# Kernel tuning notes

Measured on AMD Instinct MI355X. Metric: run time of the kernel, lower is better.

Reference implementation:

```python
import jax, jax.numpy as jnp
import numpy as np

B, T, D_MODEL = 1, 2048, 4096
NUM_Q_HEADS, NUM_KV_HEADS, KEY_SIZE = 32, 8, 128
ATTN_MULT = 0.08838834764831845  # 1/sqrt(key_size)
MAX_ATTN_VAL = 30.0


def rotate_half(x):
    x1, x2 = jnp.split(x, 2, axis=-1)
    return jnp.concatenate((-x2, x1), axis=-1)


def apply_rope(x):
    # x: [b, t, h, d]; offset = 0, positions = arange(t)
    b, t, h, d = x.shape
    exponents = jnp.arange(0, d, 2, dtype=jnp.float32)
    inv_freq = 1.0 / (10000.0 ** (exponents / d))            # [d/2]
    pos = jnp.arange(t, dtype=jnp.float32)                   # [t]
    phase = pos[:, None] * inv_freq[None, :]                 # [t, d/2]
    phase = jnp.tile(phase, (1, 2))[None, :, None, :]        # [1, t, 1, d] (tiled, not interleaved)
    return (x * jnp.cos(phase) + rotate_half(x) * jnp.sin(phase)).astype(x.dtype)


def setup_inputs() -> dict:
    key = jax.random.key(0)
    ks = jax.random.split(key, 8)
    query = jax.random.normal(ks[0], (B, T, D_MODEL), dtype=jnp.float32)
    kk = jax.random.normal(ks[1], (B, T, D_MODEL), dtype=jnp.float32)
    vv = jax.random.normal(ks[2], (B, T, D_MODEL), dtype=jnp.float32)
    mask = jnp.tril(jnp.ones((T, T), dtype=bool))[None, None, :, :]  # causal [1,1,T,T]
    s = 0.02
    Wq = jax.random.normal(ks[3], (D_MODEL, NUM_Q_HEADS * KEY_SIZE), dtype=jnp.float32) * s
    Wk = jax.random.normal(ks[4], (D_MODEL, NUM_KV_HEADS * KEY_SIZE), dtype=jnp.float32) * s
    Wv = jax.random.normal(ks[5], (D_MODEL, NUM_KV_HEADS * KEY_SIZE), dtype=jnp.float32) * s
    Wo = jax.random.normal(ks[6], (NUM_Q_HEADS * KEY_SIZE, D_MODEL), dtype=jnp.float32) * s
    return {"query": query, "key": kk, "value": vv, "mask": mask,
            "Wq": Wq, "Wk": Wk, "Wv": Wv, "Wo": Wo}


def reference(query, key, value, mask, Wq, Wk, Wv, Wo):
    b, t, _ = query.shape
    d = KEY_SIZE
    h, kv_h = NUM_Q_HEADS, NUM_KV_HEADS
    g = h // kv_h
    # projections (no bias)
    q = (query @ Wq).reshape(b, t, h, d)
    k = (key @ Wk).reshape(b, t, kv_h, d)
    v = (value @ Wv).reshape(b, t, kv_h, d)
    # RoPE on q and k
    q = apply_rope(q)
    k = apply_rope(k)
    # GQA grouping: [b, t, kv_h, g, d]
    q = q.reshape(b, t, kv_h, g, d)
    logits = jnp.einsum('btkgd,bTkd->bkgtT', q, k).astype(jnp.float32)
    logits = logits * ATTN_MULT
    logits = MAX_ATTN_VAL * jnp.tanh(logits / MAX_ATTN_VAL)  # soft-capping
    m = mask[:, :, None, :, :]  # [b,1,1,t,T]
    logits = jnp.where(m, logits, -1e30)
    weights = jax.nn.softmax(logits, axis=-1).astype(query.dtype)
    attn = jnp.einsum('bkgtT,bTkd->btkgd', weights, v)
    attn = attn.reshape(b, t, h * d)
    return attn @ Wo
```

## Files before the change

kernel.cpp:

```cpp
#include <hip/hip_runtime.h>
#include <hip/hip_bf16.h>
#include <stdint.h>
#include <stddef.h>

#define T_SEQ 2048
#define DM    4096
#define NQH   32
#define NKVH  8
#define HD    128
#define ATTN_MULT 0.08838834764831845f

typedef __attribute__((ext_vector_type(8))) short bf16x8;
typedef __attribute__((ext_vector_type(4))) float f32x4;
typedef __attribute__((ext_vector_type(4))) unsigned int u32x4;

__device__ __forceinline__ unsigned short f2b(float f) {
  unsigned u = __builtin_bit_cast(unsigned, f);
  u = u + 0x7FFFu + ((u >> 16) & 1u);
  return (unsigned short)(u >> 16);
}
__device__ __forceinline__ float b2f(unsigned short h) {
  unsigned u = ((unsigned)h) << 16;
  return __builtin_bit_cast(float, u);
}

typedef const __attribute__((address_space(1))) void* gptr1_t;
typedef __attribute__((address_space(3))) void* lptr3_t;
__device__ __forceinline__ void gl_lds16(const void* g, void* l) {
  __builtin_amdgcn_global_load_lds((gptr1_t)g, (lptr3_t)l, 16, 0, 0);
}

__global__ __launch_bounds__(256) void transpose_cast_kernel(
    const float* __restrict__ W, unsigned short* __restrict__ WT, int K, int N) {
  __shared__ float tile[64][65];
  int k0 = blockIdx.x * 64;
  int n0 = blockIdx.y * 64;
  int t = threadIdx.x;
  int rr = t >> 4;
  int cc = t & 15;
#pragma unroll
  for (int c = 0; c < 4; ++c) {
    int row = c * 16 + rr;
    float4 v = *(const float4*)&W[(size_t)(k0 + row) * N + n0 + cc * 4];
    tile[row][cc * 4 + 0] = v.x;
    tile[row][cc * 4 + 1] = v.y;
    tile[row][cc * 4 + 2] = v.z;
    tile[row][cc * 4 + 3] = v.w;
  }
  __syncthreads();
  int orow = t >> 2;
  int kb = (t & 3) * 16;
  u32x4 o1, o2;
#pragma unroll
  for (int u = 0; u < 4; ++u) {
    o1[u] = (unsigned)f2b(tile[kb + 2 * u][orow]) |
            ((unsigned)f2b(tile[kb + 2 * u + 1][orow]) << 16);
    o2[u] = (unsigned)f2b(tile[kb + 8 + 2 * u][orow]) |
            ((unsigned)f2b(tile[kb + 9 + 2 * u][orow]) << 16);
  }
  unsigned short* dst = &WT[(size_t)(n0 + orow) * K + k0 + kb];
  *(u32x4*)dst = o1;
  *(u32x4*)(dst + 8) = o2;
}

__global__ __launch_bounds__(256) void cast3_kernel(
    const float* __restrict__ a0, const float* __restrict__ a1, const float* __restrict__ a2,
    unsigned short* __restrict__ b0, unsigned short* __restrict__ b1, unsigned short* __restrict__ b2) {
  const float* in = blockIdx.z == 0 ? a0 : (blockIdx.z == 1 ? a1 : a2);
  unsigned short* out = blockIdx.z == 0 ? b0 : (blockIdx.z == 1 ? b1 : b2);
  size_t idx = ((size_t)blockIdx.x * 256 + threadIdx.x) * 8;
  float4 x = *(const float4*)(in + idx);
  float4 y = *(const float4*)(in + idx + 4);
  u32x4 v;
  v[0] = (unsigned)f2b(x.x) | ((unsigned)f2b(x.y) << 16);
  v[1] = (unsigned)f2b(x.z) | ((unsigned)f2b(x.w) << 16);
  v[2] = (unsigned)f2b(y.x) | ((unsigned)f2b(y.y) << 16);
  v[3] = (unsigned)f2b(y.z) | ((unsigned)f2b(y.w) << 16);
  *(u32x4*)(out + idx) = v;
}

template <bool F32OUT>
__device__ __forceinline__ void gemm_dp_body(
    unsigned short* lds,
    const unsigned short* __restrict__ A, const unsigned short* __restrict__ BT,
    void* __restrict__ C, int N, int K, int m0, int n0) {
  int t = threadIdx.x;
  int w = t >> 6, l = t & 63;
  int wm = w >> 2, wn = w & 3;
  int lr = l & 15, lh = l >> 4;

  f32x4 acc[4][4] = {};

  int lrow8 = l >> 3;
  int scb = ((l & 7) ^ lrow8) << 4;
  const int NT = K >> 6;

  auto stage = [&](int tt, int bsel) {
    int kb = tt * 64;
#pragma unroll
    for (int c = 0; c < 6; ++c) {
      int chunk = w * 6 + c;
      if (chunk < 16) {
        const char* src = (const char*)A +
            ((size_t)(m0 + chunk * 8 + lrow8) * K + kb) * 2 + scb;
        gl_lds16(src, (char*)lds + bsel * 49152 + chunk * 1024);
      } else {
        const char* src = (const char*)BT +
            ((size_t)(n0 + (chunk - 16) * 8 + lrow8) * K + kb) * 2 + scb;
        gl_lds16(src, (char*)lds + bsel * 49152 + 16384 + (chunk - 16) * 1024);
      }
    }
  };

  stage(0, 0);
  stage(1, 1);
  asm volatile("s_waitcnt vmcnt(6)" ::: "memory");
  __builtin_amdgcn_s_barrier();

  int bsel = 0, bnext = 2;
  for (int tt = 0; tt < NT; ++tt) {
    bool pre = (tt + 2 < NT);
    if (pre) stage(tt + 2, bnext);
    const char* Ab = (const char*)lds + bsel * 49152;
    const char* Bb = Ab + 16384;
#pragma unroll
    for (int ks = 0; ks < 2; ++ks) {
      bf16x8 af[4], bfp[4];
      int cswz = ks * 64;
#pragma unroll
      for (int i = 0; i < 4; ++i) {
        int row = wm * 64 + i * 16 + lr;
        af[i] = *(const bf16x8*)(Ab + row * 128 + ((cswz + lh * 16) ^ ((lr & 7) << 4)));
      }
#pragma unroll
      for (int j = 0; j < 4; ++j) {
        int row = wn * 64 + j * 16 + lr;
        bfp[j] = *(const bf16x8*)(Bb + row * 128 + ((cswz + lh * 16) ^ ((lr & 7) << 4)));
      }
      __builtin_amdgcn_s_setprio(1);
#pragma unroll
      for (int i = 0; i < 4; ++i)
#pragma unroll
        for (int j = 0; j < 4; ++j)
          acc[i][j] = __builtin_amdgcn_mfma_f32_16x16x32_bf16(af[i], bfp[j], acc[i][j], 0, 0, 0);
      __builtin_amdgcn_s_setprio(0);
    }
    if (pre) asm volatile("s_waitcnt vmcnt(6)" ::: "memory");
    else     asm volatile("s_waitcnt vmcnt(0)" ::: "memory");
    __builtin_amdgcn_s_barrier();
    bsel = (bsel == 2) ? 0 : bsel + 1;
    bnext = (bnext == 2) ? 0 : bnext + 1;
  }

#pragma unroll
  for (int i = 0; i < 4; ++i) {
#pragma unroll
    for (int j = 0; j < 4; ++j) {
#pragma unroll
      for (int r = 0; r < 4; ++r) {
        int row = m0 + wm * 64 + i * 16 + lh * 4 + r;
        int col = n0 + wn * 64 + j * 16 + lr;
        if constexpr (F32OUT)
          ((float*)C)[(size_t)row * N + col] = acc[i][j][r];
        else
          ((unsigned short*)C)[(size_t)row * N + col] = f2b(acc[i][j][r]);
      }
    }
  }
}

__global__ __launch_bounds__(512, 1) void qkv_dp_kernel(
    const unsigned short* __restrict__ qb, const unsigned short* __restrict__ WqT, unsigned short* __restrict__ Qp,
    const unsigned short* __restrict__ kb, const unsigned short* __restrict__ WkT, unsigned short* __restrict__ Kp,
    const unsigned short* __restrict__ vb, const unsigned short* __restrict__ WvT, unsigned short* __restrict__ Vp) {
  __shared__ unsigned short lds[3 * 24576];
  int flat = blockIdx.x;
  const unsigned short *A, *BT;
  unsigned short* C;
  int N, m0, n0;
  if (flat < 256) {
    A = qb; BT = WqT; C = Qp; N = NQH * HD;
    int xcd = flat & 7, idx = flat >> 3;
    n0 = (xcd * 2 + (idx & 1)) * 256;
    m0 = (idx >> 1) * 128;
  } else {
    int lf = flat - 256;
    int sel = lf >> 6;
    int local = lf & 63;
    A = sel ? vb : kb;
    BT = sel ? WvT : WkT;
    C = sel ? Vp : Kp;
    N = NKVH * HD;
    m0 = (local >> 2) * 128;
    n0 = (local & 3) * 256;
  }
  gemm_dp_body<false>(lds, A, BT, C, N, DM, m0, n0);
}

__global__ __launch_bounds__(512, 1) void gemm_dp_kernel(
    const unsigned short* __restrict__ A, const unsigned short* __restrict__ BT,
    float* __restrict__ C, int M, int N, int K) {
  __shared__ unsigned short lds[3 * 24576];
  int nx = gridDim.x;
  int flat = blockIdx.y * nx + blockIdx.x;
  int npx = nx >> 3;
  int xcd = flat & 7, idx = flat >> 3;
  int n0 = (xcd * npx + idx % npx) * 256;
  int m0 = (idx / npx) * 128;
  gemm_dp_body<true>(lds, A, BT, C, N, K, m0, n0);
}

__global__ __launch_bounds__(256) void sincos_kernel(float2* __restrict__ tab) {
  int idx = blockIdx.x * 256 + threadIdx.x;
  int i = idx & 63;
  int tpos = idx >> 6;
  float invf = exp2f(-(float)i * (13.287712379549449f / 64.0f));
  float phase = (float)tpos * invf;
  float s, c;
  sincosf(phase, &s, &c);
  tab[idx] = make_float2(c, s);
}

__global__ __launch_bounds__(256) void rope_kernel(unsigned short* __restrict__ X,
                                                   const float2* __restrict__ tab,
                                                   int hshift, float scale) {
  int idx = blockIdx.x * 256 + threadIdx.x;
  int i = idx & 63;
  int rest = idx >> 6;
  int nheads = 1 << hshift;
  int hh = rest & (nheads - 1);
  int tpos = rest >> hshift;
  float2 cs = tab[tpos * 64 + i];
  size_t base = (size_t)tpos * ((size_t)nheads * HD) + (size_t)hh * HD + i;
  float x1 = b2f(X[base]);
  float x2 = b2f(X[base + 64]);
  X[base] = f2b((x1 * cs.x - x2 * cs.y) * scale);
  X[base + 64] = f2b((x2 * cs.x + x1 * cs.y) * scale);
}

__global__ __launch_bounds__(256) void vtrans_kernel(
    const unsigned short* __restrict__ V, unsigned short* __restrict__ VT) {
  size_t flat = ((size_t)blockIdx.x * 256 + threadIdx.x) * 8;
  int t8 = (int)(flat & (T_SEQ - 1));
  int dh = (int)(flat >> 11);
  u32x4 v;
#pragma unroll
  for (int u = 0; u < 4; ++u) {
    unsigned short lo = V[(size_t)(t8 + 2 * u) * (NKVH * HD) + dh];
    unsigned short hi = V[(size_t)(t8 + 2 * u + 1) * (NKVH * HD) + dh];
    v[u] = (unsigned)lo | ((unsigned)hi << 16);
  }
  *(u32x4*)(VT + flat) = v;
}

template <bool DIAG>
__device__ __forceinline__ void softmax_frag(const f32x4 s[4], float& lsum, bf16x8 pf[2],
                                             int lr, int lh, int wq) {
  constexpr float C2f = (float)(-60.0 * 1.4426950408889634);
  float pv[4][4];
#pragma unroll
  for (int ct = 0; ct < 4; ++ct)
#pragma unroll
    for (int r = 0; r < 4; ++r) {
      float u = exp2f(s[ct][r]);
      float p = exp2f(C2f * __builtin_amdgcn_rcpf(u + 1.0f));
      if constexpr (DIAG) {
        int kg = ct * 16 + lh * 4 + r;
        int qg = wq * 16 + lr;
        if (kg > qg) p = 0.0f;
      }
      pv[ct][r] = p;
      lsum += p;
    }
  unsigned pk[4][2];
#pragma unroll
  for (int ct = 0; ct < 4; ++ct) {
    pk[ct][0] = (unsigned)f2b(pv[ct][0]) | ((unsigned)f2b(pv[ct][1]) << 16);
    pk[ct][1] = (unsigned)f2b(pv[ct][2]) | ((unsigned)f2b(pv[ct][3]) << 16);
  }
  int s0 = ((lh & 1) << 5) + lr;
  int s1 = s0 + 16;
  bool hi = (lh >= 2);
#pragma unroll
  for (int ks = 0; ks < 2; ++ks) {
    unsigned a0 = (unsigned)__shfl((int)pk[2 * ks][0], s0, 64);
    unsigned a1 = (unsigned)__shfl((int)pk[2 * ks][1], s0, 64);
    unsigned a2 = (unsigned)__shfl((int)pk[2 * ks][0], s1, 64);
    unsigned a3 = (unsigned)__shfl((int)pk[2 * ks][1], s1, 64);
    unsigned b0 = (unsigned)__shfl((int)pk[2 * ks + 1][0], s0, 64);
    unsigned b1 = (unsigned)__shfl((int)pk[2 * ks + 1][1], s0, 64);
    unsigned b2 = (unsigned)__shfl((int)pk[2 * ks + 1][0], s1, 64);
    unsigned b3 = (unsigned)__shfl((int)pk[2 * ks + 1][1], s1, 64);
    u32x4 f;
    f[0] = hi ? b0 : a0;
    f[1] = hi ? b1 : a1;
    f[2] = hi ? b2 : a2;
    f[3] = hi ? b3 : a3;
    pf[ks] = __builtin_bit_cast(bf16x8, f);
  }
}

template <bool WITHA, bool DIAGA, bool DIAGB>
__device__ __forceinline__ void attn_tile(
    const char* KsCur, const char* VsCur,
    const bf16x8 qfA[4], const bf16x8 qfB[4],
    f32x4 oaccA[8], f32x4 oaccB[8],
    float& lsumA, float& lsumB,
    int lr, int lh, int wq) {
  f32x4 sB[4], sA[4];
#pragma unroll
  for (int ct = 0; ct < 4; ++ct) {
    f32x4 zB = {};
    f32x4 zA = {};
#pragma unroll
    for (int kk = 0; kk < 4; ++kk) {
      int row = ct * 16 + lr;
      int cb = (kk * 32 + lh * 8) * 2;
      bf16x8 kf = *(const bf16x8*)(KsCur + row * 256 + (cb ^ ((row & 7) << 4)));
      zB = __builtin_amdgcn_mfma_f32_16x16x32_bf16(kf, qfB[kk], zB, 0, 0, 0);
      if constexpr (WITHA) zA = __builtin_amdgcn_mfma_f32_16x16x32_bf16(kf, qfA[kk], zA, 0, 0, 0);
    }
    sB[ct] = zB;
    if constexpr (WITHA) sA[ct] = zA;
  }
  bf16x8 pfB[2], pfA[2];
  softmax_frag<DIAGB>(sB, lsumB, pfB, lr, lh, wq);
  if constexpr (WITHA) softmax_frag<DIAGA>(sA, lsumA, pfA, lr, lh, wq);
#pragma unroll
  for (int ks = 0; ks < 2; ++ks) {
    int pcb = (ks * 32 + lh * 8) * 2;
#pragma unroll
    for (int dt = 0; dt < 8; ++dt) {
      int vrow = dt * 16 + lr;
      bf16x8 vf = *(const bf16x8*)(VsCur + ((vrow * 128 + pcb) ^ ((vrow & 7) << 4)));
      oaccB[dt] = __builtin_amdgcn_mfma_f32_16x16x32_bf16(pfB[ks], vf, oaccB[dt], 0, 0, 0);
      if constexpr (WITHA) oaccA[dt] = __builtin_amdgcn_mfma_f32_16x16x32_bf16(pfA[ks], vf, oaccA[dt], 0, 0, 0);
    }
  }
}

__global__ __launch_bounds__(512, 2) void attn_kernel(
    const unsigned short* __restrict__ Q,
    const unsigned short* __restrict__ Kx,
    const unsigned short* __restrict__ VT,
    unsigned short* __restrict__ O) {
  __shared__ unsigned short Ks[2][64 * 128];
  __shared__ unsigned short Vs[2][128 * 64];

  int bx = blockIdx.x;
  int by = blockIdx.y;
  int qtA = bx, qtB = 31 - bx;
  int t = threadIdx.x;
  int w = t >> 6, l = t & 63;
  int wq = w & 3;
  int hh = by * 2 + (w >> 2);
  int kvh = by >> 1;
  int lr = l & 15, lh = l >> 4;

  bf16x8 qfA[4], qfB[4];
  {
    const unsigned short* qpA = Q + (size_t)(qtA * 64 + wq * 16 + lr) * (NQH * HD) + hh * HD + lh * 8;
    const unsigned short* qpB = Q + (size_t)(qtB * 64 + wq * 16 + lr) * (NQH * HD) + hh * HD + lh * 8;
#pragma unroll
    for (int kk = 0; kk < 4; ++kk) {
      qfA[kk] = *(const bf16x8*)(qpA + kk * 32);
      qfB[kk] = *(const bf16x8*)(qpB + kk * 32);
    }
  }

  f32x4 oaccA[8] = {}, oaccB[8] = {};
  float lsumA = 0.f, lsumB = 0.f;

  const char* KgB = (const char*)Kx + (size_t)kvh * HD * 2;
  const char* VgB = (const char*)VT + (size_t)kvh * HD * T_SEQ * 2;

  auto stage = [&](int kt, int b) {
#pragma unroll
    for (int c = 0; c < 2; ++c) {
      int chunk = w * 2 + c;
      int p = chunk * 1024 + l * 16;
      {
        int row = p >> 8;
        int cb = p & 255;
        int cbl = cb ^ ((row & 7) << 4);
        gl_lds16(KgB + (size_t)(kt * 64 + row) * (NKVH * HD * 2) + cbl,
                 (char*)Ks[b] + chunk * 1024);
      }
      {
        int row = p >> 7;
        int cb = p & 127;
        int cbl = cb ^ ((row & 7) << 4);
        gl_lds16(VgB + (size_t)row * (T_SEQ * 2) + (size_t)kt * 128 + cbl,
                 (char*)Vs[b] + chunk * 1024);
      }
    }
  };

  stage(0, 0);
  __syncthreads();

  int cur = 0;
  for (int kt = 0; kt <= qtB; ++kt) {
    if (kt < qtB) stage(kt + 1, cur ^ 1);
    const char* Kc = (const char*)Ks[cur];
    const char* Vc = (const char*)Vs[cur];
    if (kt < qtA)
      attn_tile<true, false, false>(Kc, Vc, qfA, qfB, oaccA, oaccB, lsumA, lsumB, lr, lh, wq);
    else if (kt == qtA)
      attn_tile<true, true, false>(Kc, Vc, qfA, qfB, oaccA, oaccB, lsumA, lsumB, lr, lh, wq);
    else if (kt < qtB)
      attn_tile<false, false, false>(Kc, Vc, qfA, qfB, oaccA, oaccB, lsumA, lsumB, lr, lh, wq);
    else
      attn_tile<false, false, true>(Kc, Vc, qfA, qfB, oaccA, oaccB, lsumA, lsumB, lr, lh, wq);
    __syncthreads();
    cur ^= 1;
  }

  lsumB += __shfl_xor(lsumB, 16, 64);
  lsumB += __shfl_xor(lsumB, 32, 64);
  lsumA += __shfl_xor(lsumA, 16, 64);
  lsumA += __shfl_xor(lsumA, 32, 64);

#pragma unroll
  for (int i = 0; i < 4; ++i) {
    int srcl = (l & 48) | (lh * 4 + i);
    float invB = 1.0f / __shfl(lsumB, srcl, 64);
    float invA = 1.0f / __shfl(lsumA, srcl, 64);
    int qgB = qtB * 64 + wq * 16 + lh * 4 + i;
    int qgA = qtA * 64 + wq * 16 + lh * 4 + i;
#pragma unroll
    for (int dt = 0; dt < 8; ++dt) {
      O[(size_t)qgB * (NQH * HD) + hh * HD + dt * 16 + lr] = f2b(oaccB[dt][i] * invB);
      O[(size_t)qgA * (NQH * HD) + hh * HD + dt * 16 + lr] = f2b(oaccA[dt][i] * invA);
    }
  }
}

extern "C" void kernel_launch(void* const* d_in, const int* in_sizes, int n_in,
                              void* d_out, int out_size, void* d_ws, size_t ws_size,
                              hipStream_t stream) {
  const float* query = (const float*)d_in[0];
  const float* key = (const float*)d_in[1];
  const float* value = (const float*)d_in[2];
  const float* Wq = (const float*)d_in[4];
  const float* Wk = (const float*)d_in[5];
  const float* Wv = (const float*)d_in[6];
  const float* Wo = (const float*)d_in[7];
  float* out = (float*)d_out;

  char* ws = (char*)d_ws;
  constexpr size_t OFF_WQT = 0;
  constexpr size_t OFF_WOT = 33554432;
  constexpr size_t OFF_WKT = 67108864;
  constexpr size_t OFF_WVT = 75497472;
  constexpr size_t OFF_QB = 83886080;
  constexpr size_t OFF_KB = 100663296;
  constexpr size_t OFF_VB = 117440512;
  constexpr size_t OFF_QP = 134217728;
  constexpr size_t OFF_KP = 150994944;
  constexpr size_t OFF_VP = 155189248;
  constexpr size_t OFF_VT = 159383552;
  constexpr size_t OFF_AT = 163577856;
  constexpr size_t WS_NEED = 180355072;
  if (ws_size < WS_NEED) return;

  unsigned short* WqT = (unsigned short*)(ws + OFF_WQT);
  unsigned short* WoT = (unsigned short*)(ws + OFF_WOT);
  unsigned short* WkT = (unsigned short*)(ws + OFF_WKT);
  unsigned short* WvT = (unsigned short*)(ws + OFF_WVT);
  unsigned short* qb = (unsigned short*)(ws + OFF_QB);
  unsigned short* kb = (unsigned short*)(ws + OFF_KB);
  unsigned short* vb = (unsigned short*)(ws + OFF_VB);
  unsigned short* Qp = (unsigned short*)(ws + OFF_QP);
  unsigned short* Kp = (unsigned short*)(ws + OFF_KP);
  unsigned short* Vp = (unsigned short*)(ws + OFF_VP);
  unsigned short* VTb = (unsigned short*)(ws + OFF_VT);
  unsigned short* attnb = (unsigned short*)(ws + OFF_AT);
  float2* tab = (float2*)(ws + OFF_QB);

  transpose_cast_kernel<<<dim3(64, 64), 256, 0, stream>>>(Wq, WqT, DM, NQH * HD);
  transpose_cast_kernel<<<dim3(64, 16), 256, 0, stream>>>(Wk, WkT, DM, NKVH * HD);
  transpose_cast_kernel<<<dim3(64, 16), 256, 0, stream>>>(Wv, WvT, DM, NKVH * HD);
  transpose_cast_kernel<<<dim3(64, 64), 256, 0, stream>>>(Wo, WoT, NQH * HD, DM);
  cast3_kernel<<<dim3(4096, 1, 3), 256, 0, stream>>>(query, key, value, qb, kb, vb);
  qkv_dp_kernel<<<dim3(384), 512, 0, stream>>>(qb, WqT, Qp, kb, WkT, Kp, vb, WvT, Vp);
  sincos_kernel<<<dim3(T_SEQ * 64 / 256), 256, 0, stream>>>(tab);
  constexpr float C1 = (float)(0.08838834764831845 * 1.4426950408889634 / 15.0);
  rope_kernel<<<dim3(T_SEQ * NQH * 64 / 256), 256, 0, stream>>>(Qp, tab, 5, C1);
  rope_kernel<<<dim3(T_SEQ * NKVH * 64 / 256), 256, 0, stream>>>(Kp, tab, 3, 1.0f);
  vtrans_kernel<<<dim3(NKVH * HD * T_SEQ / (256 * 8)), 256, 0, stream>>>(Vp, VTb);
  attn_kernel<<<dim3(16, 16), 512, 0, stream>>>(Qp, Kp, VTb, attnb);
  gemm_dp_kernel<<<dim3(16, 16), 512, 0, stream>>>(attnb, WoT, out, T_SEQ, DM, DM);
}
```

Measured before the change: 400.9 us.

## Interleave GEMM prefetch with MFMA phases and fuse weight transpose launches

The GEMM main loop is split into four MFMA phases, each preceded by a partial LDS fragment load and one third of the next tile's global-to-LDS staging. Barriers and priority toggles bracket each phase so the waves stay in lockstep and global loads are spread across the compute. Separately, the four weight transpose-cast launches are merged into one kernel with a 2D grid that picks the matrix from blockIdx.y, removing three launches. The extra barriers per iteration add synchronization cost and could serialize waves that previously overlapped.

```diff
diff --git a/kernel.cpp b/kernel.cpp
--- a/kernel.cpp
+++ b/kernel.cpp
@@ -30,11 +30,24 @@
   __builtin_amdgcn_global_load_lds((gptr1_t)g, (lptr3_t)l, 16, 0, 0);
 }
 
-__global__ __launch_bounds__(256) void transpose_cast_kernel(
-    const float* __restrict__ W, unsigned short* __restrict__ WT, int K, int N) {
+#define MFMA16(a, b, c) __builtin_amdgcn_mfma_f32_16x16x32_bf16((a), (b), (c), 0, 0, 0)
+
+__global__ __launch_bounds__(256) void transpose_cast4_kernel(
+    const float* __restrict__ Wq, const float* __restrict__ Wk,
+    const float* __restrict__ Wv, const float* __restrict__ Wo,
+    unsigned short* __restrict__ WqT, unsigned short* __restrict__ WkT,
+    unsigned short* __restrict__ WvT, unsigned short* __restrict__ WoT) {
   __shared__ float tile[64][65];
+  int y = blockIdx.y;
+  const float* W;
+  unsigned short* WT;
+  int N, n0;
+  if (y < 64)      { W = Wq; WT = WqT; N = 4096; n0 = y * 64; }
+  else if (y < 80) { W = Wk; WT = WkT; N = 1024; n0 = (y - 64) * 64; }
+  else if (y < 96) { W = Wv; WT = WvT; N = 1024; n0 = (y - 80) * 64; }
+  else             { W = Wo; WT = WoT; N = 4096; n0 = (y - 96) * 64; }
+  const int K = 4096;
   int k0 = blockIdx.x * 64;
-  int n0 = blockIdx.y * 64;
   int t = threadIdx.x;
   int rr = t >> 4;
   int cc = t & 15;
@@ -95,11 +108,11 @@
   int scb = ((l & 7) ^ lrow8) << 4;
   const int NT = K >> 6;
 
-  auto stage = [&](int tt, int bsel) {
+  auto stage2 = [&](int tt, int bsel, int c0) {
     int kb = tt * 64;
 #pragma unroll
-    for (int c = 0; c < 6; ++c) {
-      int chunk = w * 6 + c;
+    for (int c = 0; c < 2; ++c) {
+      int chunk = w * 6 + c0 + c;
       if (chunk < 16) {
         const char* src = (const char*)A +
             ((size_t)(m0 + chunk * 8 + lrow8) * K + kb) * 2 + scb;
@@ -112,39 +125,91 @@
     }
   };
 
-  stage(0, 0);
-  stage(1, 1);
+  stage2(0, 0, 0); stage2(0, 0, 2); stage2(0, 0, 4);
+  stage2(1, 1, 0); stage2(1, 1, 2); stage2(1, 1, 4);
   asm volatile("s_waitcnt vmcnt(6)" ::: "memory");
   __builtin_amdgcn_s_barrier();
 
   int bsel = 0, bnext = 2;
   for (int tt = 0; tt < NT; ++tt) {
     bool pre = (tt + 2 < NT);
-    if (pre) stage(tt + 2, bnext);
     const char* Ab = (const char*)lds + bsel * 49152;
     const char* Bb = Ab + 16384;
-#pragma unroll
-    for (int ks = 0; ks < 2; ++ks) {
-      bf16x8 af[4], bfp[4];
-      int cswz = ks * 64;
-#pragma unroll
-      for (int i = 0; i < 4; ++i) {
-        int row = wm * 64 + i * 16 + lr;
-        af[i] = *(const bf16x8*)(Ab + row * 128 + ((cswz + lh * 16) ^ ((lr & 7) << 4)));
-      }
-#pragma unroll
-      for (int j = 0; j < 4; ++j) {
-        int row = wn * 64 + j * 16 + lr;
-        bfp[j] = *(const bf16x8*)(Bb + row * 128 + ((cswz + lh * 16) ^ ((lr & 7) << 4)));
-      }
-      __builtin_amdgcn_s_setprio(1);
-#pragma unroll
-      for (int i = 0; i < 4; ++i)
-#pragma unroll
-        for (int j = 0; j < 4; ++j)
-          acc[i][j] = __builtin_amdgcn_mfma_f32_16x16x32_bf16(af[i], bfp[j], acc[i][j], 0, 0, 0);
-      __builtin_amdgcn_s_setprio(0);
-    }
+    int rswz = (lr & 7) << 4;
+    int arow = wm * 64 + lr;
+    int brow = wn * 64 + lr;
+    int cb0 = (lh * 16) ^ rswz;
+    int cb1 = (64 + lh * 16) ^ rswz;
+
+    bf16x8 a0 = *(const bf16x8*)(Ab + (arow + 0) * 128 + cb0);
+    bf16x8 a1 = *(const bf16x8*)(Ab + (arow + 16) * 128 + cb0);
+    bf16x8 b0 = *(const bf16x8*)(Bb + (brow + 0) * 128 + cb0);
+    bf16x8 b1 = *(const bf16x8*)(Bb + (brow + 16) * 128 + cb0);
+    bf16x8 b2 = *(const bf16x8*)(Bb + (brow + 32) * 128 + cb0);
+    bf16x8 b3 = *(const bf16x8*)(Bb + (brow + 48) * 128 + cb0);
+    if (pre) stage2(tt + 2, bnext, 0);
+    __builtin_amdgcn_s_barrier();
+    __builtin_amdgcn_s_setprio(1);
+    acc[0][0] = MFMA16(a0, b0, acc[0][0]);
+    acc[0][1] = MFMA16(a0, b1, acc[0][1]);
+    acc[0][2] = MFMA16(a0, b2, acc[0][2]);
+    acc[0][3] = MFMA16(a0, b3, acc[0][3]);
+    acc[1][0] = MFMA16(a1, b0, acc[1][0]);
+    acc[1][1] = MFMA16(a1, b1, acc[1][1]);
+    acc[1][2] = MFMA16(a1, b2, acc[1][2]);
+    acc[1][3] = MFMA16(a1, b3, acc[1][3]);
+    __builtin_amdgcn_s_setprio(0);
+    __builtin_amdgcn_s_barrier();
+
+    a0 = *(const bf16x8*)(Ab + (arow + 32) * 128 + cb0);
+    a1 = *(const bf16x8*)(Ab + (arow + 48) * 128 + cb0);
+    if (pre) stage2(tt + 2, bnext, 2);
+    __builtin_amdgcn_s_barrier();
+    __builtin_amdgcn_s_setprio(1);
+    acc[2][0] = MFMA16(a0, b0, acc[2][0]);
+    acc[2][1] = MFMA16(a0, b1, acc[2][1]);
+    acc[2][2] = MFMA16(a0, b2, acc[2][2]);
+    acc[2][3] = MFMA16(a0, b3, acc[2][3]);
+    acc[3][0] = MFMA16(a1, b0, acc[3][0]);
+    acc[3][1] = MFMA16(a1, b1, acc[3][1]);
+    acc[3][2] = MFMA16(a1, b2, acc[3][2]);
+    acc[3][3] = MFMA16(a1, b3, acc[3][3]);
+    __builtin_amdgcn_s_setprio(0);
+    __builtin_amdgcn_s_barrier();
+
+    a0 = *(const bf16x8*)(Ab + (arow + 0) * 128 + cb1);
+    a1 = *(const bf16x8*)(Ab + (arow + 16) * 128 + cb1);
+    b0 = *(const bf16x8*)(Bb + (brow + 0) * 128 + cb1);
+    b1 = *(const bf16x8*)(Bb + (brow + 16) * 128 + cb1);
+    b2 = *(const bf16x8*)(Bb + (brow + 32) * 128 + cb1);
+    b3 = *(const bf16x8*)(Bb + (brow + 48) * 128 + cb1);
+    if (pre) stage2(tt + 2, bnext, 4);
+    __builtin_amdgcn_s_barrier();
+    __builtin_amdgcn_s_setprio(1);
+    acc[0][0] = MFMA16(a0, b0, acc[0][0]);
+    acc[0][1] = MFMA16(a0, b1, acc[0][1]);
+    acc[0][2] = MFMA16(a0, b2, acc[0][2]);
+    acc[0][3] = MFMA16(a0, b3, acc[0][3]);
+    acc[1][0] = MFMA16(a1, b0, acc[1][0]);
+    acc[1][1] = MFMA16(a1, b1, acc[1][1]);
+    acc[1][2] = MFMA16(a1, b2, acc[1][2]);
+    acc[1][3] = MFMA16(a1, b3, acc[1][3]);
+    __builtin_amdgcn_s_setprio(0);
+    __builtin_amdgcn_s_barrier();
+
+    a0 = *(const bf16x8*)(Ab + (arow + 32) * 128 + cb1);
+    a1 = *(const bf16x8*)(Ab + (arow + 48) * 128 + cb1);
+    __builtin_amdgcn_s_barrier();
+    __builtin_amdgcn_s_setprio(1);
+    acc[2][0] = MFMA16(a0, b0, acc[2][0]);
+    acc[2][1] = MFMA16(a0, b1, acc[2][1]);
+    acc[2][2] = MFMA16(a0, b2, acc[2][2]);
+    acc[2][3] = MFMA16(a0, b3, acc[2][3]);
+    acc[3][0] = MFMA16(a1, b0, acc[3][0]);
+    acc[3][1] = MFMA16(a1, b1, acc[3][1]);
+    acc[3][2] = MFMA16(a1, b2, acc[3][2]);
+    acc[3][3] = MFMA16(a1, b3, acc[3][3]);
+    __builtin_amdgcn_s_setprio(0);
     if (pre) asm volatile("s_waitcnt vmcnt(6)" ::: "memory");
     else     asm volatile("s_waitcnt vmcnt(0)" ::: "memory");
     __builtin_amdgcn_s_barrier();
@@ -317,8 +382,8 @@
       int row = ct * 16 + lr;
       int cb = (kk * 32 + lh * 8) * 2;
       bf16x8 kf = *(const bf16x8*)(KsCur + row * 256 + (cb ^ ((row & 7) << 4)));
-      zB = __builtin_amdgcn_mfma_f32_16x16x32_bf16(kf, qfB[kk], zB, 0, 0, 0);
-      if constexpr (WITHA) zA = __builtin_amdgcn_mfma_f32_16x16x32_bf16(kf, qfA[kk], zA, 0, 0, 0);
+      zB = MFMA16(kf, qfB[kk], zB);
+      if constexpr (WITHA) zA = MFMA16(kf, qfA[kk], zA);
     }
     sB[ct] = zB;
     if constexpr (WITHA) sA[ct] = zA;
@@ -333,8 +398,8 @@
     for (int dt = 0; dt < 8; ++dt) {
       int vrow = dt * 16 + lr;
       bf16x8 vf = *(const bf16x8*)(VsCur + ((vrow * 128 + pcb) ^ ((vrow & 7) << 4)));
-      oaccB[dt] = __builtin_amdgcn_mfma_f32_16x16x32_bf16(pfB[ks], vf, oaccB[dt], 0, 0, 0);
-      if constexpr (WITHA) oaccA[dt] = __builtin_amdgcn_mfma_f32_16x16x32_bf16(pfA[ks], vf, oaccA[dt], 0, 0, 0);
+      oaccB[dt] = MFMA16(pfB[ks], vf, oaccB[dt]);
+      if constexpr (WITHA) oaccA[dt] = MFMA16(pfA[ks], vf, oaccA[dt]);
     }
   }
 }
@@ -478,10 +543,8 @@
   unsigned short* attnb = (unsigned short*)(ws + OFF_AT);
   float2* tab = (float2*)(ws + OFF_QB);
 
-  transpose_cast_kernel<<<dim3(64, 64), 256, 0, stream>>>(Wq, WqT, DM, NQH * HD);
-  transpose_cast_kernel<<<dim3(64, 16), 256, 0, stream>>>(Wk, WkT, DM, NKVH * HD);
-  transpose_cast_kernel<<<dim3(64, 16), 256, 0, stream>>>(Wv, WvT, DM, NKVH * HD);
-  transpose_cast_kernel<<<dim3(64, 64), 256, 0, stream>>>(Wo, WoT, NQH * HD, DM);
+  transpose_cast4_kernel<<<dim3(64, 160), 256, 0, stream>>>(
+      Wq, Wk, Wv, Wo, WqT, WkT, WvT, WoT);
   cast3_kernel<<<dim3(4096, 1, 3), 256, 0, stream>>>(query, key, value, qb, kb, vb);
   qkv_dp_kernel<<<dim3(384), 512, 0, stream>>>(qb, WqT, Qp, kb, WkT, Kp, vb, WvT, Vp);
   sincos_kernel<<<dim3(T_SEQ * 64 / 256), 256, 0, stream>>>(tab);
```

New measurement: 407.2 us. Within noise of the previous version (+1.6%).
